# Kernel tuning notes

Hardware: AMD Instinct MI355X
Metric: run time of the kernel (lower is better)

Reference implementation:

```python
import jax, jax.numpy as jnp
import numpy as np

B, C, T, H, W = 1024, 1, 500, 7, 7
HID, OUT = 16, 2


def setup_inputs() -> dict:
    key = jax.random.key(0)
    k1, k2, k3, k4 = jax.random.split(key, 4)
    rppg_embeddings = jax.random.normal(k1, (B, C, T, H, W), dtype=jnp.float32)
    rBr = jax.random.normal(k2, (B, C, T), dtype=jnp.float32)
    # final_dense_layer params: Linear(500,16) -> Dropout (identity at eval) -> Linear(16,2)
    W1 = jax.random.normal(k3, (C * T, HID), dtype=jnp.float32) / np.sqrt(C * T)
    b1 = jnp.zeros((HID,), dtype=jnp.float32)
    W2 = jax.random.normal(k4, (HID, OUT), dtype=jnp.float32) / np.sqrt(HID)
    b2 = jnp.zeros((OUT,), dtype=jnp.float32)
    return {"rppg_embeddings": rppg_embeddings, "rBr": rBr,
            "W1": W1, "b1": b1, "W2": W2, "b2": b2}


def reference(rppg_embeddings, rBr, W1, b1, W2, b2):
    # AvgPool3d(kernel=[1,7,7], stride=1, pad=0) on (B,C,T,7,7) -> (B,C,T,1,1):
    # equivalent to mean over the full 7x7 spatial window.
    x = jnp.mean(rppg_embeddings, axis=(-2, -1))            # (B, C, T)
    # batched FFT phase along time (replaces the per-(b,c) Python loop)
    phase = jnp.angle(jnp.fft.fft(x, axis=-1))              # (B, C, T)
    flat = phase.reshape(phase.shape[0], -1)                # (B, C*T) = (B, 500)
    h = flat @ W1 + b1                                      # (B, 16); dropout = identity (eval)
    rBP = h @ W2 + b2                                       # (B, 2)
    return rBP
```

## Files before the change

### kernel.cpp

```cpp
#include <hip/hip_runtime.h>
#include <math.h>

#ifndef M_PI
#define M_PI 3.14159265358979323846
#endif

#define T_LEN 500
#define HW49  49
#define HID   16
#define NOUT  2

__global__ __launch_bounds__(256, 4) void bp_head_kernel(
    const float* __restrict__ rppg,
    const float* __restrict__ W1,
    const float* __restrict__ b1,
    const float* __restrict__ W2,
    const float* __restrict__ b2,
    float* __restrict__ out)
{
    __shared__ __align__(16) float stage[6272];
    __shared__ __align__(16) float xsh[T_LEN];

    const int tid = threadIdx.x;
    const int b   = blockIdx.x;
    const float* src = rppg + (size_t)b * (T_LEN * HW49);

    for (int c = 0; c < 4; ++c) {
        const int bin0 = c * 128;
        const int bins = (bin0 + 128 <= T_LEN) ? 128 : (T_LEN - bin0);
        const int nv4  = (bins * HW49) >> 2;
        const float4* s4 = (const float4*)(src + bin0 * HW49);
        float4* st4 = (float4*)stage;
        for (int i = tid; i < nv4; i += 256) st4[i] = s4[i];
        __syncthreads();
        if (tid < bins) {
            float acc = 0.f;
            const float* p = stage + tid * HW49;
            #pragma unroll
            for (int j = 0; j < HW49; ++j) acc += p[j];
            xsh[bin0 + tid] = acc * (1.0f / 49.0f);
        }
        __syncthreads();
    }

    float hp[HID];
    #pragma unroll
    for (int j = 0; j < HID; ++j) hp[j] = 0.f;

    if (tid <= 250) {
        const int k = tid;
        float ph;
        if (k == 250) {
            ph = 0.0f;
        } else {
            const double ang = (double)k * (-2.0 * M_PI / 500.0);
            double c1, s1;
            sincos(ang, &s1, &c1);
            const double c2 = fma(c1, c1, -(s1 * s1));
            const double s2 = 2.0 * c1 * s1;
            const double c4 = fma(c2, c2, -(s2 * s2));
            const double s4 = 2.0 * c2 * s2;
            const double c3 = fma(c1, c2, -(s1 * s2));
            const double s3 = fma(c1, s2,  (s1 * c2));

            double cw = 1.0, sw = 0.0;
            double re0 = 0.0, im0 = 0.0, re1 = 0.0, im1 = 0.0;
            double re2 = 0.0, im2 = 0.0, re3 = 0.0, im3 = 0.0;
            const float4* x4 = (const float4*)xsh;
            for (int j = 0; j < 125; ++j) {
                const float4 xv = x4[j];
                const double x0 = (double)xv.x, x1 = (double)xv.y;
                const double x2 = (double)xv.z, x3 = (double)xv.w;
                re0 = fma(x0, cw, re0); im0 = fma(x0, sw, im0);
                re1 = fma(x1, cw, re1); im1 = fma(x1, sw, im1);
                re2 = fma(x2, cw, re2); im2 = fma(x2, sw, im2);
                re3 = fma(x3, cw, re3); im3 = fma(x3, sw, im3);
                const double tc = fma(cw, c4, -(sw * s4));
                sw = fma(cw, s4, sw * c4);
                cw = tc;
            }
            const double re = re0 + (fma(c1, re1, -(s1 * im1)))
                                  + (fma(c2, re2, -(s2 * im2)))
                                  + (fma(c3, re3, -(s3 * im3)));
            const double im = im0 + (fma(c1, im1,  (s1 * re1)))
                                  + (fma(c2, im2,  (s2 * re2)))
                                  + (fma(c3, im3,  (s3 * re3)));
            ph = (float)atan2(im, re);
        }

        if (k == 0 || k == 250) {
            const float* w = W1 + k * HID;
            #pragma unroll
            for (int j = 0; j < HID; ++j) hp[j] = ph * w[j];
        } else {
            const float* wa = W1 + k * HID;
            const float* wb = W1 + (T_LEN - k) * HID;
            #pragma unroll
            for (int j = 0; j < HID; ++j) hp[j] = ph * (wa[j] - wb[j]);
        }
    }

    __syncthreads();
    float* hred = stage;
    #pragma unroll
    for (int j = 0; j < HID; ++j) hred[tid * 17 + j] = hp[j];
    __syncthreads();
    for (int sft = 128; sft >= 1; sft >>= 1) {
        if (tid < sft) {
            #pragma unroll
            for (int j = 0; j < HID; ++j)
                hred[tid * 17 + j] += hred[(tid + sft) * 17 + j];
        }
        __syncthreads();
    }

    if (tid < NOUT) {
        const int o = tid;
        float acc = b2[o];
        #pragma unroll
        for (int j = 0; j < HID; ++j)
            acc = fmaf(hred[j] + b1[j], W2[j * NOUT + o], acc);
        out[b * NOUT + o] = acc;
    }
}

extern "C" void kernel_launch(void* const* d_in, const int* in_sizes, int n_in,
                              void* d_out, int out_size, void* d_ws, size_t ws_size,
                              hipStream_t stream) {
    const float* rppg = (const float*)d_in[0];
    const float* W1 = (const float*)d_in[2];
    const float* b1 = (const float*)d_in[3];
    const float* W2 = (const float*)d_in[4];
    const float* b2 = (const float*)d_in[5];
    float* out = (float*)d_out;

    bp_head_kernel<<<dim3(1024), dim3(256), 0, stream>>>(rppg, W1, b1, W2, b2, out);
}
```

Measured before the change: 173.7 us.

## Split pooling and DFT head into separate kernels via workspace

Splits the fused kernel into a pooling kernel with 4096 blocks (one per row and time chunk) that writes the pooled series to workspace, and a DFT/head kernel that reads it back. The DFT kernel holds the series in shared memory as doubles, which removes per-iteration float-to-double conversions. The intent is more parallelism and better memory-level overlap in the bandwidth-heavy pooling stage. The cost is an extra launch and a workspace round trip. The old fused kernel stays as a fallback when the workspace is too small.

```diff
diff --git a/kernel.cpp b/kernel.cpp
--- a/kernel.cpp
+++ b/kernel.cpp
@@ -10,38 +10,46 @@
 #define HID   16
 #define NOUT  2
 
-__global__ __launch_bounds__(256, 4) void bp_head_kernel(
-    const float* __restrict__ rppg,
+__global__ __launch_bounds__(256) void pool_kernel(
+    const float* __restrict__ rppg, float* __restrict__ xout)
+{
+    __shared__ __align__(16) float stage[6272];
+    const int tid   = threadIdx.x;
+    const int row   = blockIdx.x >> 2;
+    const int chunk = blockIdx.x & 3;
+    const int bin0  = chunk * 128;
+    const int bins  = (bin0 + 128 <= T_LEN) ? 128 : (T_LEN - bin0);
+    const int nv4   = (bins * HW49) >> 2;
+    const float* src = rppg + (size_t)row * (T_LEN * HW49) + bin0 * HW49;
+    const float4* s4 = (const float4*)src;
+    float4* st4 = (float4*)stage;
+    for (int i = tid; i < nv4; i += 256) st4[i] = s4[i];
+    __syncthreads();
+    if (tid < bins) {
+        float acc = 0.f;
+        const float* p = stage + tid * HW49;
+        #pragma unroll
+        for (int j = 0; j < HW49; ++j) acc += p[j];
+        xout[row * T_LEN + bin0 + tid] = acc * (1.0f / 49.0f);
+    }
+}
+
+__global__ __launch_bounds__(256, 4) void dft_head_kernel(
+    const float* __restrict__ xin,
     const float* __restrict__ W1,
     const float* __restrict__ b1,
     const float* __restrict__ W2,
     const float* __restrict__ b2,
     float* __restrict__ out)
 {
-    __shared__ __align__(16) float stage[6272];
-    __shared__ __align__(16) float xsh[T_LEN];
-
+    __shared__ __align__(16) double xd[T_LEN];
+    __shared__ float hred[256 * 17];
     const int tid = threadIdx.x;
-    const int b   = blockIdx.x;
-    const float* src = rppg + (size_t)b * (T_LEN * HW49);
-
-    for (int c = 0; c < 4; ++c) {
-        const int bin0 = c * 128;
-        const int bins = (bin0 + 128 <= T_LEN) ? 128 : (T_LEN - bin0);
-        const int nv4  = (bins * HW49) >> 2;
-        const float4* s4 = (const float4*)(src + bin0 * HW49);
-        float4* st4 = (float4*)stage;
-        for (int i = tid; i < nv4; i += 256) st4[i] = s4[i];
-        __syncthreads();
-        if (tid < bins) {
-            float acc = 0.f;
-            const float* p = stage + tid * HW49;
-            #pragma unroll
-            for (int j = 0; j < HW49; ++j) acc += p[j];
-            xsh[bin0 + tid] = acc * (1.0f / 49.0f);
-        }
-        __syncthreads();
-    }
+    const int row = blockIdx.x;
+
+    const float* xr = xin + (size_t)row * T_LEN;
+    for (int i = tid; i < T_LEN; i += 256) xd[i] = (double)xr[i];
+    __syncthreads();
 
     float hp[HID];
     #pragma unroll
@@ -66,14 +74,121 @@
             double cw = 1.0, sw = 0.0;
             double re0 = 0.0, im0 = 0.0, re1 = 0.0, im1 = 0.0;
             double re2 = 0.0, im2 = 0.0, re3 = 0.0, im3 = 0.0;
+            const double2* x2 = (const double2*)xd;
+            for (int j = 0; j < 125; ++j) {
+                const double2 xa = x2[2 * j];
+                const double2 xb = x2[2 * j + 1];
+                re0 = fma(xa.x, cw, re0); im0 = fma(xa.x, sw, im0);
+                re1 = fma(xa.y, cw, re1); im1 = fma(xa.y, sw, im1);
+                re2 = fma(xb.x, cw, re2); im2 = fma(xb.x, sw, im2);
+                re3 = fma(xb.y, cw, re3); im3 = fma(xb.y, sw, im3);
+                const double tc = fma(cw, c4, -(sw * s4));
+                sw = fma(cw, s4, sw * c4);
+                cw = tc;
+            }
+            const double re = re0 + (fma(c1, re1, -(s1 * im1)))
+                                  + (fma(c2, re2, -(s2 * im2)))
+                                  + (fma(c3, re3, -(s3 * im3)));
+            const double im = im0 + (fma(c1, im1,  (s1 * re1)))
+                                  + (fma(c2, im2,  (s2 * re2)))
+                                  + (fma(c3, im3,  (s3 * re3)));
+            ph = (float)atan2(im, re);
+        }
+
+        if (k == 0 || k == 250) {
+            const float* w = W1 + k * HID;
+            #pragma unroll
+            for (int j = 0; j < HID; ++j) hp[j] = ph * w[j];
+        } else {
+            const float* wa = W1 + k * HID;
+            const float* wb = W1 + (T_LEN - k) * HID;
+            #pragma unroll
+            for (int j = 0; j < HID; ++j) hp[j] = ph * (wa[j] - wb[j]);
+        }
+    }
+
+    __syncthreads();
+    #pragma unroll
+    for (int j = 0; j < HID; ++j) hred[tid * 17 + j] = hp[j];
+    __syncthreads();
+    for (int sft = 128; sft >= 1; sft >>= 1) {
+        if (tid < sft) {
+            #pragma unroll
+            for (int j = 0; j < HID; ++j)
+                hred[tid * 17 + j] += hred[(tid + sft) * 17 + j];
+        }
+        __syncthreads();
+    }
+
+    if (tid < NOUT) {
+        const int o = tid;
+        float acc = b2[o];
+        #pragma unroll
+        for (int j = 0; j < HID; ++j)
+            acc = fmaf(hred[j] + b1[j], W2[j * NOUT + o], acc);
+        out[row * NOUT + o] = acc;
+    }
+}
+
+__global__ __launch_bounds__(256, 4) void bp_head_fused_kernel(
+    const float* __restrict__ rppg,
+    const float* __restrict__ W1, const float* __restrict__ b1,
+    const float* __restrict__ W2, const float* __restrict__ b2,
+    float* __restrict__ out)
+{
+    __shared__ __align__(16) float stage[6272];
+    __shared__ __align__(16) float xsh[T_LEN];
+    const int tid = threadIdx.x;
+    const int b   = blockIdx.x;
+    const float* src = rppg + (size_t)b * (T_LEN * HW49);
+
+    for (int c = 0; c < 4; ++c) {
+        const int bin0 = c * 128;
+        const int bins = (bin0 + 128 <= T_LEN) ? 128 : (T_LEN - bin0);
+        const int nv4  = (bins * HW49) >> 2;
+        const float4* s4 = (const float4*)(src + bin0 * HW49);
+        float4* st4 = (float4*)stage;
+        for (int i = tid; i < nv4; i += 256) st4[i] = s4[i];
+        __syncthreads();
+        if (tid < bins) {
+            float acc = 0.f;
+            const float* p = stage + tid * HW49;
+            #pragma unroll
+            for (int j = 0; j < HW49; ++j) acc += p[j];
+            xsh[bin0 + tid] = acc * (1.0f / 49.0f);
+        }
+        __syncthreads();
+    }
+
+    float hp[HID];
+    #pragma unroll
+    for (int j = 0; j < HID; ++j) hp[j] = 0.f;
+
+    if (tid <= 250) {
+        const int k = tid;
+        float ph;
+        if (k == 250) {
+            ph = 0.0f;
+        } else {
+            const double ang = (double)k * (-2.0 * M_PI / 500.0);
+            double c1, s1;
+            sincos(ang, &s1, &c1);
+            const double c2 = fma(c1, c1, -(s1 * s1));
+            const double s2 = 2.0 * c1 * s1;
+            const double c4 = fma(c2, c2, -(s2 * s2));
+            const double s4 = 2.0 * c2 * s2;
+            const double c3 = fma(c1, c2, -(s1 * s2));
+            const double s3 = fma(c1, s2,  (s1 * c2));
+            double cw = 1.0, sw = 0.0;
+            double re0 = 0, im0 = 0, re1 = 0, im1 = 0, re2 = 0, im2 = 0, re3 = 0, im3 = 0;
             const float4* x4 = (const float4*)xsh;
             for (int j = 0; j < 125; ++j) {
                 const float4 xv = x4[j];
                 const double x0 = (double)xv.x, x1 = (double)xv.y;
-                const double x2 = (double)xv.z, x3 = (double)xv.w;
+                const double x2v = (double)xv.z, x3 = (double)xv.w;
                 re0 = fma(x0, cw, re0); im0 = fma(x0, sw, im0);
                 re1 = fma(x1, cw, re1); im1 = fma(x1, sw, im1);
-                re2 = fma(x2, cw, re2); im2 = fma(x2, sw, im2);
+                re2 = fma(x2v, cw, re2); im2 = fma(x2v, sw, im2);
                 re3 = fma(x3, cw, re3); im3 = fma(x3, sw, im3);
                 const double tc = fma(cw, c4, -(sw * s4));
                 sw = fma(cw, s4, sw * c4);
@@ -87,7 +202,6 @@
                                   + (fma(c3, im3,  (s3 * re3)));
             ph = (float)atan2(im, re);
         }
-
         if (k == 0 || k == 250) {
             const float* w = W1 + k * HID;
             #pragma unroll
@@ -113,7 +227,6 @@
         }
         __syncthreads();
     }
-
     if (tid < NOUT) {
         const int o = tid;
         float acc = b2[o];
@@ -134,5 +247,12 @@
     const float* b2 = (const float*)d_in[5];
     float* out = (float*)d_out;
 
-    bp_head_kernel<<<dim3(1024), dim3(256), 0, stream>>>(rppg, W1, b1, W2, b2, out);
-}
+    const size_t need = (size_t)1024 * T_LEN * sizeof(float);
+    if (ws_size >= need) {
+        float* x = (float*)d_ws;
+        pool_kernel<<<dim3(4096), dim3(256), 0, stream>>>(rppg, x);
+        dft_head_kernel<<<dim3(1024), dim3(256), 0, stream>>>(x, W1, b1, W2, b2, out);
+    } else {
+        bp_head_fused_kernel<<<dim3(1024), dim3(256), 0, stream>>>(rppg, W1, b1, W2, b2, out);
+    }
+}
```

Result: no change. 174.7 us (+0.5%).
